# Kernel tuning notes

Measured on AMD Instinct MI355X. Metric: run time of the kernel, lower is better.

The kernel has to match this reference:

```python
import jax, jax.numpy as jnp
import numpy as np

S, N, L, D, H, V = 64, 128, 10, 300, 150, 50000


def setup_inputs() -> dict:
    key = jax.random.key(0)
    k0, k1, k2, k3 = jax.random.split(key, 4)
    tokens = jax.random.randint(k0, (S, N), 0, V)
    emb_table = jax.random.normal(k1, (V, D), jnp.float32) * 0.02
    W1 = jax.random.normal(k2, (D, H), jnp.float32) * (1.0 / np.sqrt(D))
    b1 = jnp.zeros((H,), jnp.float32)
    W2 = jax.random.normal(k3, (H, 1), jnp.float32) * (1.0 / np.sqrt(H))
    b2 = jnp.zeros((1,), jnp.float32)
    return {"tokens": tokens, "emb_table": emb_table, "W1": W1, "b1": b1, "W2": W2, "b2": b2}


def reference(tokens, emb_table, W1, b1, W2, b2):
    # word embeddings per sentence: [S, N, D]
    emb = emb_table[tokens]
    # FFNN attention score per token: Linear->ReLU->Linear(->1), squeeze -> [S, N]
    scores = (jax.nn.relu(emb @ W1 + b1) @ W2 + b2)[..., 0]

    n = tokens.shape[1]
    k = jnp.arange(L)                      # window position within span
    pos = jnp.arange(n)
    idx = pos[:, None] + k[None, :]        # [N, L] absolute token index of span (i, i+k)
    valid = idx < n                        # span position in-bounds
    idx_c = jnp.minimum(idx, n - 1)

    win_emb = emb[:, idx_c]                # [S, N, L, D]  emb[s, i+k]
    win_sc = scores[:, idx_c]              # [S, N, L]     scores[s, i+k]

    # tri[w, k] = (k <= w): positions belonging to span of width index w
    tri = k[:, None] >= k[None, :]                       # [L, L]
    m = tri[None, None] & valid[None, :, None, :]        # [1, N, L(w), L(k)]
    logits = jnp.where(m, win_sc[:, :, None, :], -jnp.inf)
    probs = jax.nn.softmax(logits, axis=-1)              # [S, N, Lw, Lk]
    head = jnp.einsum('snwk,snkd->snwd', probs, win_emb)  # softmax-weighted sum

    first = jnp.broadcast_to(emb[:, :, None, :], win_emb.shape)  # emb[i]
    last = win_emb                                               # emb[i+w] at k-axis == w
    out = jnp.concatenate([first, last, head], axis=-1)          # [S, N, L, 3D]
    # zero out spans that run past the sentence end
    return out * valid[None, :, :, None].astype(out.dtype)
```

## Files before the change

### kernel.cpp

```cpp
#include <hip/hip_runtime.h>
#include <cstddef>

#define SS 64
#define NN 128
#define LL 10
#define DD 300
#define HH 150
#define HP 160

#define WS_EMB 0
#define WS_SC  (SS*NN*DD)
#define WS_W1P (WS_SC + SS*NN)
#define WS_BW  (WS_W1P + DD*HP)

__device__ __forceinline__ void fma4(float4& a, float s, const float4 b) {
    a.x = fmaf(s, b.x, a.x);
    a.y = fmaf(s, b.y, a.y);
    a.z = fmaf(s, b.z, a.z);
    a.w = fmaf(s, b.w, a.w);
}

__global__ void pad_weights(const float* __restrict__ W1, const float* __restrict__ b1,
                            const float* __restrict__ W2, float* __restrict__ W1p,
                            float* __restrict__ bW) {
    int idx = blockIdx.x * 256 + threadIdx.x;
    if (idx < DD * HP) {
        int d = idx / HP, j = idx - d * HP;
        W1p[idx] = (j < HH) ? W1[d * HH + j] : 0.f;
    }
    if (idx < HP) {
        bW[idx] = (idx < HH) ? b1[idx] : 0.f;
    } else if (idx < 2 * HP) {
        int j = idx - HP;
        bW[idx] = (j < HH) ? W2[j] : 0.f;
    }
}

constexpr int TB = 32;

__global__ __launch_bounds__(256) void k_emb_scores(
        const int* __restrict__ tokens, const float* __restrict__ table,
        const float* __restrict__ W1p, const float* __restrict__ bW,
        const float* __restrict__ b2,
        float* __restrict__ ws_emb, float* __restrict__ ws_sc)
{
    __shared__ float lemb[TB][DD + 4];
    __shared__ float lpart[TB][40];
    __shared__ int   ltok[TB];

    const int tid = threadIdx.x;
    const int t0  = blockIdx.x * TB;

    if (tid < TB) ltok[tid] = tokens[t0 + tid];
    __syncthreads();

    for (int l = tid; l < TB * 75; l += 256) {
        const int t = l / 75, q = l - t * 75;
        const float4 v = *(const float4*)(table + (size_t)ltok[t] * DD + q * 4);
        *(float4*)&lemb[t][q * 4] = v;
        *(float4*)(ws_emb + (size_t)(t0 + t) * DD + q * 4) = v;
    }
    __syncthreads();

    for (int slot = tid; slot < 8 * 38; slot += 256) {
        const int tg = slot / 38;
        const int jg = slot - tg * 38;
        const int j0 = jg * 4;
        const int tt = tg * 4;

        float4 acc0 = {0,0,0,0}, acc1 = {0,0,0,0}, acc2 = {0,0,0,0}, acc3 = {0,0,0,0};
        const float* wp = W1p + j0;

        #pragma unroll 5
        for (int d = 0; d < DD; d += 4) {
            const float4 e0 = *(const float4*)&lemb[tt + 0][d];
            const float4 e1 = *(const float4*)&lemb[tt + 1][d];
            const float4 e2 = *(const float4*)&lemb[tt + 2][d];
            const float4 e3 = *(const float4*)&lemb[tt + 3][d];
            const float4 w0 = *(const float4*)(wp + (size_t)(d + 0) * HP);
            const float4 w1 = *(const float4*)(wp + (size_t)(d + 1) * HP);
            const float4 w2 = *(const float4*)(wp + (size_t)(d + 2) * HP);
            const float4 w3 = *(const float4*)(wp + (size_t)(d + 3) * HP);
            fma4(acc0, e0.x, w0); fma4(acc0, e0.y, w1); fma4(acc0, e0.z, w2); fma4(acc0, e0.w, w3);
            fma4(acc1, e1.x, w0); fma4(acc1, e1.y, w1); fma4(acc1, e1.z, w2); fma4(acc1, e1.w, w3);
            fma4(acc2, e2.x, w0); fma4(acc2, e2.y, w1); fma4(acc2, e2.z, w2); fma4(acc2, e2.w, w3);
            fma4(acc3, e3.x, w0); fma4(acc3, e3.y, w1); fma4(acc3, e3.z, w2); fma4(acc3, e3.w, w3);
        }

        const float4 bb = *(const float4*)(bW + j0);
        const float4 v2 = *(const float4*)(bW + HP + j0);

        #define RELD(A) (fmaxf((A).x + bb.x, 0.f) * v2.x + \
                         fmaxf((A).y + bb.y, 0.f) * v2.y + \
                         fmaxf((A).z + bb.z, 0.f) * v2.z + \
                         fmaxf((A).w + bb.w, 0.f) * v2.w)
        lpart[tt + 0][jg] = RELD(acc0);
        lpart[tt + 1][jg] = RELD(acc1);
        lpart[tt + 2][jg] = RELD(acc2);
        lpart[tt + 3][jg] = RELD(acc3);
        #undef RELD
    }
    __syncthreads();

    if (tid < TB) {
        float s = 0.f;
        #pragma unroll
        for (int jg = 0; jg < 38; ++jg) s += lpart[tid][jg];
        ws_sc[t0 + tid] = s + b2[0];
    }
}

__global__ __launch_bounds__(256) void k_out(
        const float* __restrict__ ws_emb, const float* __restrict__ ws_sc,
        float* __restrict__ out)
{
    const int bid = blockIdx.x;
    const int i   = bid & (NN - 1);
    const int nk  = min(LL, NN - i);

    __shared__ float le[LL][DD + 4];
    __shared__ float lp[LL][12];

    const int tid = threadIdx.x;

    const float* src = ws_emb + (size_t)bid * DD;
    for (int l = tid; l < nk * 75; l += 256) {
        const int k = l / 75, q = l - k * 75;
        *(float4*)&le[k][q * 4] = *(const float4*)(src + l * 4);
    }

    if (tid < nk) {
        const int w = tid;
        const float* scp = ws_sc + bid;
        float m = -1e30f;
        for (int k = 0; k <= w; ++k) m = fmaxf(m, scp[k]);
        float sum = 0.f;
        for (int k = 0; k <= w; ++k) {
            const float e = __expf(scp[k] - m);
            lp[w][k] = e;
            sum += e;
        }
        const float inv = 1.f / sum;
        for (int k = 0; k <= w; ++k) lp[w][k] *= inv;
    }
    __syncthreads();

    float* dst = out + (size_t)bid * (LL * 3 * DD);
    for (int o4 = tid; o4 < (LL * 3 * DD) / 4; o4 += 256) {
        const int w  = o4 / 225;
        const int c4 = o4 - w * 225;
        const int c  = c4 * 4;
        float4 v;
        if (w >= nk) {
            v = make_float4(0.f, 0.f, 0.f, 0.f);
        } else if (c < DD) {
            v = *(const float4*)&le[0][c];
        } else if (c < 2 * DD) {
            v = *(const float4*)&le[w][c - DD];
        } else {
            const int cc = c - 2 * DD;
            float4 a = make_float4(0.f, 0.f, 0.f, 0.f);
            for (int k = 0; k <= w; ++k) {
                const float p = lp[w][k];
                fma4(a, p, *(const float4*)&le[k][cc]);
            }
            v = a;
        }
        *(float4*)(dst + (size_t)o4 * 4) = v;
    }
}

extern "C" void kernel_launch(void* const* d_in, const int* in_sizes, int n_in,
                              void* d_out, int out_size, void* d_ws, size_t ws_size,
                              hipStream_t stream) {
    const int*   tokens = (const int*)d_in[0];
    const float* table  = (const float*)d_in[1];
    const float* W1     = (const float*)d_in[2];
    const float* b1     = (const float*)d_in[3];
    const float* W2     = (const float*)d_in[4];
    const float* b2     = (const float*)d_in[5];
    float* out = (float*)d_out;
    float* ws  = (float*)d_ws;

    float* ws_emb = ws + WS_EMB;
    float* ws_sc  = ws + WS_SC;
    float* W1p    = ws + WS_W1P;
    float* bW     = ws + WS_BW;

    pad_weights<<<(DD * HP + 255) / 256, 256, 0, stream>>>(W1, b1, W2, W1p, bW);
    k_emb_scores<<<(SS * NN) / TB, 256, 0, stream>>>(tokens, table, W1p, bW, b2, ws_emb, ws_sc);
    k_out<<<SS * NN, 256, 0, stream>>>(ws_emb, ws_sc, out);
}
```

Baseline: 122.8 us.

## Tile output kernel over 16 positions and gather embeddings directly from table

The intermediate embedding workspace is removed: the scores kernel no longer writes gathered embeddings, and the output kernel gathers rows straight from the embedding table. Each output block now covers 16 consecutive start positions plus a 9-row halo, so every embedding row is loaded once per tile instead of up to ten times across overlapping windows. This cuts global read and write traffic, in exchange for fewer, larger blocks with more shared memory (about 30KB) and lower occupancy.

```diff
diff --git a/kernel.cpp b/kernel.cpp
--- a/kernel.cpp
+++ b/kernel.cpp
@@ -7,9 +7,10 @@
 #define DD 300
 #define HH 150
 #define HP 160
+#define CC 16
+#define RMAX (CC + LL - 1)
 
-#define WS_EMB 0
-#define WS_SC  (SS*NN*DD)
+#define WS_SC  0
 #define WS_W1P (WS_SC + SS*NN)
 #define WS_BW  (WS_W1P + DD*HP)
 
@@ -38,11 +39,10 @@
 
 constexpr int TB = 32;
 
-__global__ __launch_bounds__(256) void k_emb_scores(
+__global__ __launch_bounds__(256) void k_scores(
         const int* __restrict__ tokens, const float* __restrict__ table,
         const float* __restrict__ W1p, const float* __restrict__ bW,
-        const float* __restrict__ b2,
-        float* __restrict__ ws_emb, float* __restrict__ ws_sc)
+        const float* __restrict__ b2, float* __restrict__ ws_sc)
 {
     __shared__ float lemb[TB][DD + 4];
     __shared__ float lpart[TB][40];
@@ -56,9 +56,7 @@
 
     for (int l = tid; l < TB * 75; l += 256) {
         const int t = l / 75, q = l - t * 75;
-        const float4 v = *(const float4*)(table + (size_t)ltok[t] * DD + q * 4);
-        *(float4*)&lemb[t][q * 4] = v;
-        *(float4*)(ws_emb + (size_t)(t0 + t) * DD + q * 4) = v;
+        *(float4*)&lemb[t][q * 4] = *(const float4*)(table + (size_t)ltok[t] * DD + q * 4);
     }
     __syncthreads();
 
@@ -111,58 +109,63 @@
 }
 
 __global__ __launch_bounds__(256) void k_out(
-        const float* __restrict__ ws_emb, const float* __restrict__ ws_sc,
-        float* __restrict__ out)
+        const int* __restrict__ tokens, const float* __restrict__ table,
+        const float* __restrict__ ws_sc, float* __restrict__ out)
 {
     const int bid = blockIdx.x;
-    const int i   = bid & (NN - 1);
-    const int nk  = min(LL, NN - i);
+    const int s   = bid >> 3;
+    const int i0  = (bid & 7) * CC;
+    const int R   = min(RMAX, NN - i0);
 
-    __shared__ float le[LL][DD + 4];
-    __shared__ float lp[LL][12];
+    __shared__ float le[RMAX][DD + 4];
+    __shared__ float lp[CC][LL][12];
+    __shared__ float sc_l[RMAX];
 
     const int tid = threadIdx.x;
 
-    const float* src = ws_emb + (size_t)bid * DD;
-    for (int l = tid; l < nk * 75; l += 256) {
+    if (tid < R) sc_l[tid] = ws_sc[s * NN + i0 + tid];
+
+    const int* tk = tokens + s * NN + i0;
+    for (int l = tid; l < R * 75; l += 256) {
         const int k = l / 75, q = l - k * 75;
-        *(float4*)&le[k][q * 4] = *(const float4*)(src + l * 4);
-    }
-
-    if (tid < nk) {
-        const int w = tid;
-        const float* scp = ws_sc + bid;
-        float m = -1e30f;
-        for (int k = 0; k <= w; ++k) m = fmaxf(m, scp[k]);
-        float sum = 0.f;
-        for (int k = 0; k <= w; ++k) {
-            const float e = __expf(scp[k] - m);
-            lp[w][k] = e;
-            sum += e;
-        }
-        const float inv = 1.f / sum;
-        for (int k = 0; k <= w; ++k) lp[w][k] *= inv;
+        *(float4*)&le[k][q * 4] = *(const float4*)(table + (size_t)tk[k] * DD + q * 4);
     }
     __syncthreads();
 
-    float* dst = out + (size_t)bid * (LL * 3 * DD);
-    for (int o4 = tid; o4 < (LL * 3 * DD) / 4; o4 += 256) {
-        const int w  = o4 / 225;
-        const int c4 = o4 - w * 225;
+    if (tid < CC * LL) {
+        const int li = tid / LL, w = tid - li * LL;
+        const int nk = min(LL, NN - (i0 + li));
+        if (w < nk) {
+            float m = -1e30f;
+            for (int k = 0; k <= w; ++k) m = fmaxf(m, sc_l[li + k]);
+            float sum = 0.f;
+            for (int k = 0; k <= w; ++k) sum += __expf(sc_l[li + k] - m);
+            const float inv = 1.f / sum;
+            for (int k = 0; k <= w; ++k) lp[li][w][k] = __expf(sc_l[li + k] - m) * inv;
+        }
+    }
+    __syncthreads();
+
+    float* dst = out + (size_t)(s * NN + i0) * (LL * 3 * DD);
+    for (int o4 = tid; o4 < CC * 2250; o4 += 256) {
+        const int li = o4 / 2250;
+        const int r  = o4 - li * 2250;
+        const int w  = r / 225;
+        const int c4 = r - w * 225;
         const int c  = c4 * 4;
+        const int nk = min(LL, NN - (i0 + li));
         float4 v;
         if (w >= nk) {
             v = make_float4(0.f, 0.f, 0.f, 0.f);
         } else if (c < DD) {
-            v = *(const float4*)&le[0][c];
+            v = *(const float4*)&le[li][c];
         } else if (c < 2 * DD) {
-            v = *(const float4*)&le[w][c - DD];
+            v = *(const float4*)&le[li + w][c - DD];
         } else {
             const int cc = c - 2 * DD;
             float4 a = make_float4(0.f, 0.f, 0.f, 0.f);
             for (int k = 0; k <= w; ++k) {
-                const float p = lp[w][k];
-                fma4(a, p, *(const float4*)&le[k][cc]);
+                fma4(a, lp[li][w][k], *(const float4*)&le[li + k][cc]);
             }
             v = a;
         }
@@ -182,12 +185,11 @@
     float* out = (float*)d_out;
     float* ws  = (float*)d_ws;
 
-    float* ws_emb = ws + WS_EMB;
-    float* ws_sc  = ws + WS_SC;
-    float* W1p    = ws + WS_W1P;
-    float* bW     = ws + WS_BW;
+    float* ws_sc = ws + WS_SC;
+    float* W1p   = ws + WS_W1P;
+    float* bW    = ws + WS_BW;
 
     pad_weights<<<(DD * HP + 255) / 256, 256, 0, stream>>>(W1, b1, W2, W1p, bW);
-    k_emb_scores<<<(SS * NN) / TB, 256, 0, stream>>>(tokens, table, W1p, bW, b2, ws_emb, ws_sc);
-    k_out<<<SS * NN, 256, 0, stream>>>(ws_emb, ws_sc, out);
+    k_scores<<<(SS * NN) / TB, 256, 0, stream>>>(tokens, table, W1p, bW, b2, ws_sc);
+    k_out<<<SS * (NN / CC), 256, 0, stream>>>(tokens, table, ws_sc, out);
 }
```

After: 116.5 us. 1.05x faster.
